# Performance work log

Hardware: AMD Instinct MI355X
Metric: run time of the kernel (lower is better)

Reference implementation:

```python
import jax, jax.numpy as jnp
import numpy as np

NUM_HEADING_BIN = 12
NUM_SIZE_CLUSTER = 8
DELTA_NORM_W = 0.01
CENTER_W = 0.5
B, N = 4096, 2048


def huber(err, delta=1.0):
    a = jnp.abs(err)
    q = jnp.minimum(a, delta)
    return jnp.mean(0.5 * q * q + delta * (a - q))


def box3d_corners(centers, headings, sizes):
    # centers (B,3), headings (B,), sizes (B,3) -> (B,8,3)
    l, w, h = sizes[:, 0:1], sizes[:, 1:2], sizes[:, 2:3]
    sx = jnp.asarray([1, 1, -1, -1, 1, 1, -1, -1], dtype=sizes.dtype)
    sy = jnp.asarray([1, -1, -1, 1, 1, -1, -1, 1], dtype=sizes.dtype)
    sz = jnp.asarray([1, 1, 1, 1, -1, -1, -1, -1], dtype=sizes.dtype)
    corners = jnp.stack([0.5 * l * sx, 0.5 * w * sy, 0.5 * h * sz], axis=1)  # (B,3,8)
    c, s = jnp.cos(headings), jnp.sin(headings)
    z, o = jnp.zeros_like(c), jnp.ones_like(c)
    R = jnp.stack([jnp.stack([c, -s, z], -1),
                   jnp.stack([s, c, z], -1),
                   jnp.stack([z, z, o], -1)], axis=1)  # (B,3,3)
    out = jnp.einsum('bij,bjk->bik', R, corners) + centers[:, :, None]
    return jnp.transpose(out, (0, 2, 1))  # (B,8,3)


def setup_inputs() -> dict:
    key = jax.random.key(0)
    ks = jax.random.split(key, 9)
    return {
        'mask_xyz_mean': jax.random.normal(ks[0], (B, 3), jnp.float32),
        'point_cloud': jax.random.normal(ks[1], (B, 3, N), jnp.float32),
        'x_delta': jax.random.normal(ks[2], (B, 3, N), jnp.float32),
        'center_label': jax.random.normal(ks[3], (B, 3), jnp.float32),
        'size_residual_label': jax.random.normal(ks[4], (B, 3), jnp.float32),
        'heading_residual_label': jax.random.normal(ks[5], (B,), jnp.float32),
        'mean_sizes': jax.random.uniform(ks[6], (NUM_SIZE_CLUSTER, 3), jnp.float32, 0.5, 2.5),
        'size_class_label': jax.random.randint(ks[7], (B,), 0, NUM_SIZE_CLUSTER, jnp.int32),
        'heading_class_label': jax.random.randint(ks[8], (B,), 0, NUM_HEADING_BIN, jnp.int32),
    }


def reference(mask_xyz_mean, point_cloud, x_delta, center_label,
              size_residual_label, heading_residual_label, mean_sizes,
              size_class_label, heading_class_label):
    eps = 0.0  # faithful: original has no eps
    # center loss
    center_dist = jnp.linalg.norm(mask_xyz_mean - center_label, axis=1)
    center_loss = CENTER_W * huber(center_dist)

    # label assembly (onehot-sum == gather)
    size_label = mean_sizes[size_class_label] + size_residual_label  # (B,3)
    bin_centers = jnp.arange(0, np.pi, np.pi / NUM_HEADING_BIN, dtype=jnp.float32)
    heading_label = heading_residual_label + bin_centers[heading_class_label]  # (B,)

    corners_3d_gt = box3d_corners(center_label, heading_label, size_label)
    corners_2d_gt = corners_3d_gt[:, 4:8, :2]  # (B,4,2)

    v = center_label[:, :2]  # (B,2)
    p_dir = jnp.stack([-v[:, 1], v[:, 0]], axis=1)
    p_dir = p_dir / jnp.linalg.norm(p_dir, axis=1, keepdims=True)  # (B,2)

    pp_label = jnp.einsum('bkc,bc->bk', corners_2d_gt, p_dir)  # (B,4)
    py_max, py_min = jnp.max(pp_label, axis=1), jnp.min(pp_label, axis=1)
    std_y_label = (py_max - py_min) / 4
    mean_y_label = (py_max + py_min) / 2

    v_norm = jnp.linalg.norm(v, axis=1, keepdims=True)  # (B,1)
    proj_label = jnp.einsum('bkc,bc->bk', corners_2d_gt, v) / v_norm  # (B,4)
    p_max, p_min = jnp.max(proj_label, axis=1), jnp.min(proj_label, axis=1)
    std_label = (p_max - p_min) / 4
    mean_label = (p_max + p_min) / 2

    pc_xy = jnp.transpose(point_cloud, (0, 2, 1))[:, :, :2]  # (B,N,2)

    pp_pc = jnp.einsum('bnc,bc->bn', pc_xy, p_dir)  # (B,N)
    std_y_pc = jnp.std(pp_pc, axis=1, ddof=1)
    mean_y_pc = jnp.mean(pp_pc, axis=1)
    y_std_loss = huber(jnp.abs(std_y_label - std_y_pc))
    y_mean_loss = huber(jnp.abs(mean_y_label - mean_y_pc))

    proj_pc = jnp.einsum('bnc,bc->bn', pc_xy, v) / v_norm  # (B,N)
    std_pc = jnp.std(proj_pc, axis=1, ddof=1)
    mean_pc = jnp.mean(proj_pc, axis=1)
    x_std_loss = huber(jnp.abs(std_label - std_pc))
    x_mean_loss = huber(jnp.abs(mean_label - mean_pc))

    delta_norm = jnp.sqrt(jnp.sum(x_delta * x_delta, axis=(1, 2)))
    delta_norm_loss = DELTA_NORM_W * huber(delta_norm)

    total = center_loss + x_std_loss + x_mean_loss + delta_norm_loss + y_mean_loss + y_std_loss
    return 0.4 * total
```

## Files before the change

### kernel.cpp

```cpp
#include <hip/hip_runtime.h>
#include <math.h>

#define B_SZ 4096
#define N_PTS 2048
#define BLOCK 256

__device__ __forceinline__ float huber1(float a) {
    float q = fminf(a, 1.0f);
    return 0.5f * q * q + (a - q);
}

__global__ __launch_bounds__(BLOCK) void loss_stage1(
    const float* __restrict__ mask_xyz_mean,
    const float* __restrict__ point_cloud,
    const float* __restrict__ x_delta,
    const float* __restrict__ center_label,
    const float* __restrict__ size_residual,
    const float* __restrict__ heading_residual,
    const float* __restrict__ mean_sizes,
    const int*   __restrict__ size_class,
    const int*   __restrict__ heading_class,
    float* __restrict__ ws)
{
    const int b   = blockIdx.x;
    const int tid = threadIdx.x;

    const float cx = center_label[b * 3 + 0];
    const float cy = center_label[b * 3 + 1];

    const float vnorm2 = cx * cx + cy * cy;
    const float vnorm  = sqrtf(vnorm2);
    const float pdx = -cy / vnorm;
    const float pdy =  cx / vnorm;

    const size_t base = (size_t)b * 3 * N_PTS;
    const float4* px4 = (const float4*)(point_cloud + base);
    const float4* py4 = (const float4*)(point_cloud + base + N_PTS);
    const float4* pd4 = (const float4*)(x_delta + base);

    float s_pp = 0.f, s_pp2 = 0.f, s_t = 0.f, s_t2 = 0.f, s_d2 = 0.f;

    #pragma unroll
    for (int k = 0; k < N_PTS / 4 / BLOCK; ++k) {
        const int i = tid + k * BLOCK;
        const float4 x4 = px4[i];
        const float4 y4 = py4[i];
        {
            float pp = x4.x * pdx + y4.x * pdy;
            float t  = x4.x * cx  + y4.x * cy;
            s_pp += pp; s_pp2 += pp * pp; s_t += t; s_t2 += t * t;
        }
        {
            float pp = x4.y * pdx + y4.y * pdy;
            float t  = x4.y * cx  + y4.y * cy;
            s_pp += pp; s_pp2 += pp * pp; s_t += t; s_t2 += t * t;
        }
        {
            float pp = x4.z * pdx + y4.z * pdy;
            float t  = x4.z * cx  + y4.z * cy;
            s_pp += pp; s_pp2 += pp * pp; s_t += t; s_t2 += t * t;
        }
        {
            float pp = x4.w * pdx + y4.w * pdy;
            float t  = x4.w * cx  + y4.w * cy;
            s_pp += pp; s_pp2 += pp * pp; s_t += t; s_t2 += t * t;
        }
    }

    #pragma unroll
    for (int k = 0; k < 3 * N_PTS / 4 / BLOCK; ++k) {
        const int i = tid + k * BLOCK;
        const float4 d = pd4[i];
        s_d2 += d.x * d.x + d.y * d.y + d.z * d.z + d.w * d.w;
    }

    #pragma unroll
    for (int off = 32; off > 0; off >>= 1) {
        s_pp  += __shfl_down(s_pp,  off, 64);
        s_pp2 += __shfl_down(s_pp2, off, 64);
        s_t   += __shfl_down(s_t,   off, 64);
        s_t2  += __shfl_down(s_t2,  off, 64);
        s_d2  += __shfl_down(s_d2,  off, 64);
    }

    __shared__ float red[BLOCK / 64][5];
    const int wave = tid >> 6;
    const int lane = tid & 63;
    if (lane == 0) {
        red[wave][0] = s_pp;  red[wave][1] = s_pp2;
        red[wave][2] = s_t;   red[wave][3] = s_t2;
        red[wave][4] = s_d2;
    }
    __syncthreads();

    if (tid == 0) {
        #pragma unroll
        for (int w = 1; w < BLOCK / 64; ++w) {
            s_pp  += red[w][0];
            s_pp2 += red[w][1];
            s_t   += red[w][2];
            s_t2  += red[w][3];
            s_d2  += red[w][4];
        }

        const float mx = mask_xyz_mean[b * 3 + 0];
        const float my = mask_xyz_mean[b * 3 + 1];
        const float mz = mask_xyz_mean[b * 3 + 2];
        const float cz = center_label[b * 3 + 2];
        const float dxc = mx - cx, dyc = my - cy, dzc = mz - cz;
        const float center_dist = sqrtf(dxc * dxc + dyc * dyc + dzc * dzc);

        const int sc = size_class[b];
        const float l  = mean_sizes[sc * 3 + 0] + size_residual[b * 3 + 0];
        const float w_ = mean_sizes[sc * 3 + 1] + size_residual[b * 3 + 1];

        const float theta = heading_residual[b] +
                            (float)heading_class[b] * (float)(M_PI / 12.0);
        const float c = cosf(theta);
        const float s = sinf(theta);
        const float hl = 0.5f * l, hw = 0.5f * w_;

        float X[4], Y[4];
        X[0] =  c * hl - s * hw + cx;  Y[0] =  s * hl + c * hw + cy;
        X[1] =  c * hl + s * hw + cx;  Y[1] =  s * hl - c * hw + cy;
        X[2] = -c * hl + s * hw + cx;  Y[2] = -s * hl - c * hw + cy;
        X[3] = -c * hl - s * hw + cx;  Y[3] = -s * hl + c * hw + cy;

        float ppmax = -INFINITY, ppmin = INFINITY;
        float pmax  = -INFINITY, pmin  = INFINITY;
        #pragma unroll
        for (int k = 0; k < 4; ++k) {
            const float pp = X[k] * pdx + Y[k] * pdy;
            const float pj = (X[k] * cx + Y[k] * cy) / vnorm;
            ppmax = fmaxf(ppmax, pp); ppmin = fminf(ppmin, pp);
            pmax  = fmaxf(pmax,  pj); pmin  = fminf(pmin,  pj);
        }
        const float std_y_label  = (ppmax - ppmin) * 0.25f;
        const float mean_y_label = (ppmax + ppmin) * 0.5f;
        const float std_label    = (pmax - pmin) * 0.25f;
        const float mean_label   = (pmax + pmin) * 0.5f;

        const float invN   = 1.0f / (float)N_PTS;
        const float invNm1 = 1.0f / (float)(N_PTS - 1);

        const float mean_y_pc = s_pp * invN;
        const float var_y = (s_pp2 - s_pp * s_pp * invN) * invNm1;
        const float std_y_pc = sqrtf(fmaxf(var_y, 0.0f));

        const float mean_pc = (s_t * invN) / vnorm;
        const float var_x = ((s_t2 - s_t * s_t * invN) * invNm1) / vnorm2;
        const float std_pc = sqrtf(fmaxf(var_x, 0.0f));

        const float delta_norm = sqrtf(s_d2);

        const float total =
              0.5f  * huber1(center_dist)
            +         huber1(fabsf(std_label  - std_pc))
            +         huber1(fabsf(mean_label - mean_pc))
            + 0.01f * huber1(delta_norm)
            +         huber1(fabsf(mean_y_label - mean_y_pc))
            +         huber1(fabsf(std_y_label  - std_y_pc));

        ws[b] = total;
    }
}

__global__ __launch_bounds__(BLOCK) void loss_stage2(
    const float* __restrict__ ws, float* __restrict__ out)
{
    const int tid = threadIdx.x;
    const float4* w4 = (const float4*)ws;

    float s = 0.f;
    #pragma unroll
    for (int k = 0; k < B_SZ / 4 / BLOCK; ++k) {
        const float4 v = w4[tid + k * BLOCK];
        s += v.x + v.y + v.z + v.w;
    }

    #pragma unroll
    for (int off = 32; off > 0; off >>= 1)
        s += __shfl_down(s, off, 64);

    __shared__ float red[BLOCK / 64];
    const int wave = tid >> 6;
    const int lane = tid & 63;
    if (lane == 0) red[wave] = s;
    __syncthreads();

    if (tid == 0) {
        #pragma unroll
        for (int w = 1; w < BLOCK / 64; ++w) s += red[w];
        out[0] = s * (0.4f / (float)B_SZ);
    }
}

extern "C" void kernel_launch(void* const* d_in, const int* in_sizes, int n_in,
                              void* d_out, int out_size, void* d_ws, size_t ws_size,
                              hipStream_t stream) {
    const float* mask_xyz_mean    = (const float*)d_in[0];
    const float* point_cloud      = (const float*)d_in[1];
    const float* x_delta          = (const float*)d_in[2];
    const float* center_label     = (const float*)d_in[3];
    const float* size_residual    = (const float*)d_in[4];
    const float* heading_residual = (const float*)d_in[5];
    const float* mean_sizes       = (const float*)d_in[6];
    const int*   size_class       = (const int*)d_in[7];
    const int*   heading_class    = (const int*)d_in[8];
    float* ws  = (float*)d_ws;
    float* out = (float*)d_out;

    loss_stage1<<<B_SZ, BLOCK, 0, stream>>>(
        mask_xyz_mean, point_cloud, x_delta, center_label, size_residual,
        heading_residual, mean_sizes, size_class, heading_class, ws);
    loss_stage2<<<1, BLOCK, 0, stream>>>(ws, out);
}
```

Measured before the change: 223.7 us.

## Assign one wavefront per batch row instead of one block per row

Each 64-lane wavefront now processes a full batch item, with four items per 256-thread block, so the grid shrinks by four. This removes the shared-memory cross-wave reduction and the __syncthreads, and launch_bounds now requests 4 blocks per CU. Each lane now issues more loads (8 point and 24 delta float4s per lane), which adds register pressure and longer per-wave serial tails.

```diff
diff --git a/kernel.cpp b/kernel.cpp
--- a/kernel.cpp
+++ b/kernel.cpp
@@ -4,13 +4,14 @@
 #define B_SZ 4096
 #define N_PTS 2048
 #define BLOCK 256
+#define WPB (BLOCK / 64)
 
 __device__ __forceinline__ float huber1(float a) {
     float q = fminf(a, 1.0f);
     return 0.5f * q * q + (a - q);
 }
 
-__global__ __launch_bounds__(BLOCK) void loss_stage1(
+__global__ __launch_bounds__(BLOCK, 4) void loss_stage1(
     const float* __restrict__ mask_xyz_mean,
     const float* __restrict__ point_cloud,
     const float* __restrict__ x_delta,
@@ -22,8 +23,9 @@
     const int*   __restrict__ heading_class,
     float* __restrict__ ws)
 {
-    const int b   = blockIdx.x;
-    const int tid = threadIdx.x;
+    const int wave = threadIdx.x >> 6;
+    const int lane = threadIdx.x & 63;
+    const int b    = blockIdx.x * WPB + wave;
 
     const float cx = center_label[b * 3 + 0];
     const float cy = center_label[b * 3 + 1];
@@ -41,8 +43,8 @@
     float s_pp = 0.f, s_pp2 = 0.f, s_t = 0.f, s_t2 = 0.f, s_d2 = 0.f;
 
     #pragma unroll
-    for (int k = 0; k < N_PTS / 4 / BLOCK; ++k) {
-        const int i = tid + k * BLOCK;
+    for (int k = 0; k < N_PTS / 4 / 64; ++k) {
+        const int i = lane + k * 64;
         const float4 x4 = px4[i];
         const float4 y4 = py4[i];
         {
@@ -68,9 +70,8 @@
     }
 
     #pragma unroll
-    for (int k = 0; k < 3 * N_PTS / 4 / BLOCK; ++k) {
-        const int i = tid + k * BLOCK;
-        const float4 d = pd4[i];
+    for (int k = 0; k < 3 * N_PTS / 4 / 64; ++k) {
+        const float4 d = pd4[lane + k * 64];
         s_d2 += d.x * d.x + d.y * d.y + d.z * d.z + d.w * d.w;
     }
 
@@ -83,26 +84,7 @@
         s_d2  += __shfl_down(s_d2,  off, 64);
     }
 
-    __shared__ float red[BLOCK / 64][5];
-    const int wave = tid >> 6;
-    const int lane = tid & 63;
     if (lane == 0) {
-        red[wave][0] = s_pp;  red[wave][1] = s_pp2;
-        red[wave][2] = s_t;   red[wave][3] = s_t2;
-        red[wave][4] = s_d2;
-    }
-    __syncthreads();
-
-    if (tid == 0) {
-        #pragma unroll
-        for (int w = 1; w < BLOCK / 64; ++w) {
-            s_pp  += red[w][0];
-            s_pp2 += red[w][1];
-            s_t   += red[w][2];
-            s_t2  += red[w][3];
-            s_d2  += red[w][4];
-        }
-
         const float mx = mask_xyz_mean[b * 3 + 0];
         const float my = mask_xyz_mean[b * 3 + 1];
         const float mz = mask_xyz_mean[b * 3 + 2];
@@ -210,7 +192,7 @@
     float* ws  = (float*)d_ws;
     float* out = (float*)d_out;
 
-    loss_stage1<<<B_SZ, BLOCK, 0, stream>>>(
+    loss_stage1<<<B_SZ / WPB, BLOCK, 0, stream>>>(
         mask_xyz_mean, point_cloud, x_delta, center_label, size_residual,
         heading_residual, mean_sizes, size_class, heading_class, ws);
     loss_stage2<<<1, BLOCK, 0, stream>>>(ws, out);
```

After: 225.3 us. Within noise of the previous version (+0.7%).

## Split fused loss kernel into point-cloud stats and x_delta/epilogue kernels

Applied to the files above, without the earlier changes.

Splits the single per-sample kernel into two: one reduces the x/y point-cloud channels into four moments written to workspace, and a second reduces x_delta's squared norm and then runs the per-sample epilogue using those moments. Both kernels issue all their float4 loads up front and use a launch-bounds occupancy hint of 8 blocks. The aim is more memory-level parallelism per thread and lighter register pressure per kernel on this bandwidth-bound reduction. In exchange it adds an extra kernel launch and a small workspace round trip for the intermediate sums.

```diff
diff --git a/kernel.cpp b/kernel.cpp
--- a/kernel.cpp
+++ b/kernel.cpp
@@ -10,10 +10,77 @@
     return 0.5f * q * q + (a - q);
 }
 
-__global__ __launch_bounds__(BLOCK) void loss_stage1(
+
+__global__ __launch_bounds__(BLOCK, 8) void pc_stats(
+    const float* __restrict__ point_cloud,
+    const float* __restrict__ center_label,
+    float* __restrict__ ws)
+{
+    const int b   = blockIdx.x;
+    const int tid = threadIdx.x;
+
+    const float cx = center_label[b * 3 + 0];
+    const float cy = center_label[b * 3 + 1];
+    const float vnorm = sqrtf(cx * cx + cy * cy);
+    const float pdx = -cy / vnorm;
+    const float pdy =  cx / vnorm;
+
+    const size_t base = (size_t)b * 3 * N_PTS;
+    const float4* px4 = (const float4*)(point_cloud + base);
+    const float4* py4 = (const float4*)(point_cloud + base + N_PTS);
+
+    const float4 vx0 = px4[tid];
+    const float4 vx1 = px4[tid + BLOCK];
+    const float4 vy0 = py4[tid];
+    const float4 vy1 = py4[tid + BLOCK];
+
+    float s_pp = 0.f, s_pp2 = 0.f, s_t = 0.f, s_t2 = 0.f;
+    {
+        const float xs[8] = {vx0.x, vx0.y, vx0.z, vx0.w, vx1.x, vx1.y, vx1.z, vx1.w};
+        const float ys[8] = {vy0.x, vy0.y, vy0.z, vy0.w, vy1.x, vy1.y, vy1.z, vy1.w};
+        #pragma unroll
+        for (int j = 0; j < 8; ++j) {
+            const float pp = xs[j] * pdx + ys[j] * pdy;
+            const float t  = xs[j] * cx  + ys[j] * cy;
+            s_pp += pp; s_pp2 += pp * pp; s_t += t; s_t2 += t * t;
+        }
+    }
+
+    #pragma unroll
+    for (int off = 32; off > 0; off >>= 1) {
+        s_pp  += __shfl_down(s_pp,  off, 64);
+        s_pp2 += __shfl_down(s_pp2, off, 64);
+        s_t   += __shfl_down(s_t,   off, 64);
+        s_t2  += __shfl_down(s_t2,  off, 64);
+    }
+
+    __shared__ float red[BLOCK / 64][4];
+    const int wave = tid >> 6;
+    const int lane = tid & 63;
+    if (lane == 0) {
+        red[wave][0] = s_pp;  red[wave][1] = s_pp2;
+        red[wave][2] = s_t;   red[wave][3] = s_t2;
+    }
+    __syncthreads();
+
+    if (tid == 0) {
+        #pragma unroll
+        for (int w = 1; w < BLOCK / 64; ++w) {
+            s_pp  += red[w][0];
+            s_pp2 += red[w][1];
+            s_t   += red[w][2];
+            s_t2  += red[w][3];
+        }
+        ws[0 * B_SZ + b] = s_pp;
+        ws[1 * B_SZ + b] = s_pp2;
+        ws[2 * B_SZ + b] = s_t;
+        ws[3 * B_SZ + b] = s_t2;
+    }
+}
+
+__global__ __launch_bounds__(BLOCK, 8) void xd_epilogue(
+    const float* __restrict__ x_delta,
     const float* __restrict__ mask_xyz_mean,
-    const float* __restrict__ point_cloud,
-    const float* __restrict__ x_delta,
     const float* __restrict__ center_label,
     const float* __restrict__ size_residual,
     const float* __restrict__ heading_residual,
@@ -25,88 +92,48 @@
     const int b   = blockIdx.x;
     const int tid = threadIdx.x;
 
-    const float cx = center_label[b * 3 + 0];
-    const float cy = center_label[b * 3 + 1];
-
-    const float vnorm2 = cx * cx + cy * cy;
-    const float vnorm  = sqrtf(vnorm2);
-    const float pdx = -cy / vnorm;
-    const float pdy =  cx / vnorm;
-
-    const size_t base = (size_t)b * 3 * N_PTS;
-    const float4* px4 = (const float4*)(point_cloud + base);
-    const float4* py4 = (const float4*)(point_cloud + base + N_PTS);
-    const float4* pd4 = (const float4*)(x_delta + base);
-
-    float s_pp = 0.f, s_pp2 = 0.f, s_t = 0.f, s_t2 = 0.f, s_d2 = 0.f;
-
-    #pragma unroll
-    for (int k = 0; k < N_PTS / 4 / BLOCK; ++k) {
-        const int i = tid + k * BLOCK;
-        const float4 x4 = px4[i];
-        const float4 y4 = py4[i];
-        {
-            float pp = x4.x * pdx + y4.x * pdy;
-            float t  = x4.x * cx  + y4.x * cy;
-            s_pp += pp; s_pp2 += pp * pp; s_t += t; s_t2 += t * t;
-        }
-        {
-            float pp = x4.y * pdx + y4.y * pdy;
-            float t  = x4.y * cx  + y4.y * cy;
-            s_pp += pp; s_pp2 += pp * pp; s_t += t; s_t2 += t * t;
-        }
-        {
-            float pp = x4.z * pdx + y4.z * pdy;
-            float t  = x4.z * cx  + y4.z * cy;
-            s_pp += pp; s_pp2 += pp * pp; s_t += t; s_t2 += t * t;
-        }
-        {
-            float pp = x4.w * pdx + y4.w * pdy;
-            float t  = x4.w * cx  + y4.w * cy;
-            s_pp += pp; s_pp2 += pp * pp; s_t += t; s_t2 += t * t;
-        }
-    }
-
-    #pragma unroll
-    for (int k = 0; k < 3 * N_PTS / 4 / BLOCK; ++k) {
-        const int i = tid + k * BLOCK;
-        const float4 d = pd4[i];
-        s_d2 += d.x * d.x + d.y * d.y + d.z * d.z + d.w * d.w;
-    }
-
-    #pragma unroll
-    for (int off = 32; off > 0; off >>= 1) {
-        s_pp  += __shfl_down(s_pp,  off, 64);
-        s_pp2 += __shfl_down(s_pp2, off, 64);
-        s_t   += __shfl_down(s_t,   off, 64);
-        s_t2  += __shfl_down(s_t2,  off, 64);
-        s_d2  += __shfl_down(s_d2,  off, 64);
-    }
-
-    __shared__ float red[BLOCK / 64][5];
+    const float4* pd4 = (const float4*)(x_delta + (size_t)b * 3 * N_PTS);
+
+    float4 d[6];
+    #pragma unroll
+    for (int k = 0; k < 6; ++k)
+        d[k] = pd4[tid + k * BLOCK];
+
+    float s_d2 = 0.f;
+    #pragma unroll
+    for (int k = 0; k < 6; ++k)
+        s_d2 += d[k].x * d[k].x + d[k].y * d[k].y + d[k].z * d[k].z + d[k].w * d[k].w;
+
+    #pragma unroll
+    for (int off = 32; off > 0; off >>= 1)
+        s_d2 += __shfl_down(s_d2, off, 64);
+
+    __shared__ float red[BLOCK / 64];
     const int wave = tid >> 6;
     const int lane = tid & 63;
-    if (lane == 0) {
-        red[wave][0] = s_pp;  red[wave][1] = s_pp2;
-        red[wave][2] = s_t;   red[wave][3] = s_t2;
-        red[wave][4] = s_d2;
-    }
+    if (lane == 0) red[wave] = s_d2;
     __syncthreads();
 
     if (tid == 0) {
         #pragma unroll
-        for (int w = 1; w < BLOCK / 64; ++w) {
-            s_pp  += red[w][0];
-            s_pp2 += red[w][1];
-            s_t   += red[w][2];
-            s_t2  += red[w][3];
-            s_d2  += red[w][4];
-        }
+        for (int w = 1; w < BLOCK / 64; ++w) s_d2 += red[w];
+
+        const float s_pp  = ws[0 * B_SZ + b];
+        const float s_pp2 = ws[1 * B_SZ + b];
+        const float s_t   = ws[2 * B_SZ + b];
+        const float s_t2  = ws[3 * B_SZ + b];
+
+        const float cx = center_label[b * 3 + 0];
+        const float cy = center_label[b * 3 + 1];
+        const float cz = center_label[b * 3 + 2];
+        const float vnorm2 = cx * cx + cy * cy;
+        const float vnorm  = sqrtf(vnorm2);
+        const float pdx = -cy / vnorm;
+        const float pdy =  cx / vnorm;
 
         const float mx = mask_xyz_mean[b * 3 + 0];
         const float my = mask_xyz_mean[b * 3 + 1];
         const float mz = mask_xyz_mean[b * 3 + 2];
-        const float cz = center_label[b * 3 + 2];
         const float dxc = mx - cx, dyc = my - cy, dzc = mz - cz;
         const float center_dist = sqrtf(dxc * dxc + dyc * dyc + dzc * dzc);
 
@@ -161,15 +188,15 @@
             +         huber1(fabsf(mean_y_label - mean_y_pc))
             +         huber1(fabsf(std_y_label  - std_y_pc));
 
-        ws[b] = total;
-    }
-}
-
-__global__ __launch_bounds__(BLOCK) void loss_stage2(
+        ws[4 * B_SZ + b] = total;
+    }
+}
+
+__global__ __launch_bounds__(BLOCK) void loss_reduce(
     const float* __restrict__ ws, float* __restrict__ out)
 {
     const int tid = threadIdx.x;
-    const float4* w4 = (const float4*)ws;
+    const float4* w4 = (const float4*)(ws + 4 * B_SZ);
 
     float s = 0.f;
     #pragma unroll
@@ -210,8 +237,9 @@
     float* ws  = (float*)d_ws;
     float* out = (float*)d_out;
 
-    loss_stage1<<<B_SZ, BLOCK, 0, stream>>>(
-        mask_xyz_mean, point_cloud, x_delta, center_label, size_residual,
+    pc_stats<<<B_SZ, BLOCK, 0, stream>>>(point_cloud, center_label, ws);
+    xd_epilogue<<<B_SZ, BLOCK, 0, stream>>>(
+        x_delta, mask_xyz_mean, center_label, size_residual,
         heading_residual, mean_sizes, size_class, heading_class, ws);
-    loss_stage2<<<1, BLOCK, 0, stream>>>(ws, out);
-}
+    loss_reduce<<<1, BLOCK, 0, stream>>>(ws, out);
+}
```

Measured after the change: 223.9 us. No clear change (+0.1%).
